# Optimization experiments

Hardware: AMD Instinct MI355X
Metric: run time of the kernel (lower is better)

Reference implementation:

```python
import jax, jax.numpy as jnp
import numpy as np

T, B, D, H = 512, 128, 512, 512

def setup_inputs() -> dict:
    key = jax.random.key(0)
    k1, k2, k3, k4 = jax.random.split(key, 4)
    s_in = 1.0 / np.sqrt(D)
    s_h = 1.0 / np.sqrt(H)
    return {
        "x": jax.random.normal(k1, (T, B, D), dtype=jnp.float32),
        "resets": jax.random.randint(k2, (T, B), 0, 2) > 0,
        "h0": jnp.zeros((B, H), dtype=jnp.float32),  # GRUCell.initialize_carry -> zeros
        "Wi": jax.random.normal(k3, (D, 3 * H), dtype=jnp.float32) * s_in,  # [ir|iz|in]
        "bi": jnp.zeros((3 * H,), dtype=jnp.float32),
        "Wh": jax.random.normal(k4, (H, 3 * H), dtype=jnp.float32) * s_h,  # [hr|hz|hn]
        "bhn": jnp.zeros((H,), dtype=jnp.float32),
    }

def reference(x, resets, h0, Wi, bi, Wh, bhn):
    # Precompute all input-side gate projections in one big GEMM: [T,B,3H]
    xg = jnp.einsum('tbd,dk->tbk', x, Wi) + bi

    def step(h, inp):
        xg_t, reset_t = inp
        # reset masking: replace carry with fresh zero carry where episode resets
        h = jnp.where(reset_t[:, None], jnp.zeros_like(h), h)
        hg = h @ Wh  # [B,3H]
        xr, xz, xn = jnp.split(xg_t, 3, axis=-1)
        hr, hz, hn = jnp.split(hg, 3, axis=-1)
        r = jax.nn.sigmoid(xr + hr)
        z = jax.nn.sigmoid(xz + hz)
        n = jnp.tanh(xn + r * (hn + bhn))
        h_new = (1.0 - z) * n + z * h
        return h_new, h_new

    h_final, ys = jax.lax.scan(step, h0, (xg, resets))
    return h_final, ys
```

## Files before the change

### kernel.cpp

```cpp
#include <hip/hip_runtime.h>

typedef __attribute__((ext_vector_type(4))) float f32x4;
typedef __attribute__((ext_vector_type(8))) _Float16 f16x8;
typedef __attribute__((ext_vector_type(4))) _Float16 f16x4;
typedef unsigned short u16;
typedef unsigned int u32;
typedef unsigned long long u64;

#define XGCAP 34304
#define TRASH (XGCAP - 1)

__device__ __forceinline__ float sigm(float v){ return 1.0f / (1.0f + __expf(-v)); }
__device__ __forceinline__ float tanh_fast(float v){
  v = fminf(15.0f, fmaxf(-15.0f, v));
  float e = __expf(2.0f * v);
  return (e - 1.0f) / (e + 1.0f);
}
__device__ __forceinline__ double aload(const double* p){
  return __hip_atomic_load(p, __ATOMIC_RELAXED, __HIP_MEMORY_SCOPE_AGENT);
}
__device__ __forceinline__ void astore64(u64* p, u64 v){
  __hip_atomic_store(p, v, __ATOMIC_RELAXED, __HIP_MEMORY_SCOPE_AGENT);
}

__global__ __launch_bounds__(512) void prep_lists(
    const void* __restrict__ resets_raw, const float* __restrict__ h0,
    u32* __restrict__ rows, u32* __restrict__ off, int* __restrict__ nlists,
    u32* __restrict__ succ, _Float16* __restrict__ hq)
{
  __shared__ u32 bitmap[2048];
  __shared__ u32 cnt[520];
  __shared__ u32 offs[521];
  __shared__ u32 cur[520];
  __shared__ int is_bytes, h0nz;
  const int tid = threadIdx.x;
  const int lane = tid & 63, wave = tid >> 6;
  for (int i = tid; i < 2048; i += 512) bitmap[i] = 0;
  for (int i = tid; i < 520; i += 512){ cnt[i] = 0; cur[i] = 0; }
  if (tid == 0){ is_bytes = 0; h0nz = 0; }
  for (int i = tid; i < 64; i += 512){ rows[65536 + i] = (2u << 16); succ[65536 + i] = TRASH; }
  __syncthreads();
  {
    const u32* w = (const u32*)resets_raw;
    int bad = 0;
    for (int i = tid; i < 4096; i += 512) bad |= (w[i] > 1u);
    if (bad) atomicOr(&is_bytes, 1);
  }
  {
    const u32* hw = (const u32*)h0;
    u32 o = 0;
    for (int i = tid; i < 65536; i += 512) o |= hw[i];
    if (o) atomicOr(&h0nz, 1);
  }
  __syncthreads();
  const bool h0zero = (h0nz == 0);
  if (is_bytes){
    const u32* wb = (const u32*)resets_raw;
    for (int i = tid; i < 16384; i += 512){
      u32 v = wb[i];
      u32 bits = ((v & 0xFFu) ? 1u : 0u) | (((v >> 8) & 0xFFu) ? 2u : 0u)
               | (((v >> 16) & 0xFFu) ? 4u : 0u) | (((v >> 24) & 0xFFu) ? 8u : 0u);
      if (bits) atomicOr(&bitmap[i >> 3], bits << ((i & 7) * 4));
    }
  } else {
    const u32* w = (const u32*)resets_raw;
    for (int r = 0; r < 128; ++r){
      u32 v = w[r * 512 + tid];
      u64 m = __ballot(v != 0u);
      if (lane == 0){
        int idx = r * 16 + wave * 2;
        bitmap[idx] = (u32)m; bitmap[idx + 1] = (u32)(m >> 32);
      }
    }
  }
  __syncthreads();
  if (tid < 128){
    const int b = tid;
    int depth = 0;
    for (int t = 0; t < 512; ++t){
      int pos = t * 128 + b;
      bool rs = (bitmap[pos >> 5] >> (pos & 31)) & 1u;
      depth = rs ? 0 : ((t == 0) ? 0 : depth + 1);
      int li = (depth == 0) ? ((rs || h0zero) ? 0 : 1) : (depth + 1);
      atomicAdd(&cnt[li], 1u);
    }
  }
  __syncthreads();
  if (tid == 0){
    u32 s = 0; int mx = 0;
    for (int i = 0; i < 520; ++i){
      offs[i] = s; s += cnt[i];
      if (cnt[i]) mx = i;
    }
    offs[520] = s;
    *nlists = mx + 1;
  }
  __syncthreads();
  for (int i = tid; i < 521; i += 512) off[i] = offs[i];
  __syncthreads();
  const u32 n0 = offs[1];
  if (tid < 128){
    const int b = tid;
    int depth = 0;
    u32 prev_p = 0;
    for (int t = 0; t < 512; ++t){
      int pos = t * 128 + b;
      bool rs = (bitmap[pos >> 5] >> (pos & 31)) & 1u;
      depth = rs ? 0 : ((t == 0) ? 0 : depth + 1);
      int li = (depth == 0) ? ((rs || h0zero) ? 0 : 1) : (depth + 1);
      u32 p = offs[li] + atomicAdd(&cur[li], 1u);
      u32 fl = rs ? 1u : ((t == 0) ? (h0zero ? 1u : 2u) : 0u);
      rows[p] = (u32)t | ((u32)b << 9) | (fl << 16);
      succ[p] = TRASH;
      if (t > 0 && !rs) succ[prev_p] = p - n0;
      prev_p = p;
    }
  }
  __syncthreads();
  if (!h0zero){
    const u32 c1 = offs[2] - offs[1];
    for (u32 idx = tid; idx < c1 * 512u; idx += 512){
      u32 lpos = offs[1] + (idx >> 9);
      u32 c = idx & 511u;
      u32 b = (rows[lpos] >> 9) & 127u;
      hq[(size_t)(lpos - n0) * 512 + c] = (_Float16)h0[(size_t)b * 512 + c];
    }
  }
}

__global__ void prep_w(const float* __restrict__ Wi, const float* __restrict__ Wh,
                       char* __restrict__ wimg, u32* __restrict__ flags)
{
  if (blockIdx.x < 64){
    #pragma unroll
    for (int i = 0; i < 4; ++i)
      flags[blockIdx.x * 1024 + (int)threadIdx.x + i * 256] = 0;
  }
  __shared__ float tile[64][65];
  const int bc = blockIdx.x % 24;
  const int bk = blockIdx.x / 24;
  const int scol0 = (bc % 3) * 512 + (bc / 3) * 64;
  const int k0 = bk * 64;
  #pragma unroll
  for (int i = 0; i < 4; ++i){
    int idx = (int)threadIdx.x + i*256;
    int kk = idx >> 4, c4 = idx & 15;
    int k = k0 + kk;
    const float* src = (k < 512) ? (Wi + (size_t)k*1536 + scol0 + c4*4)
                                 : (Wh + (size_t)(k-512)*1536 + scol0 + c4*4);
    float4 v = *(const float4*)src;
    tile[kk][c4*4+0] = v.x; tile[kk][c4*4+1] = v.y;
    tile[kk][c4*4+2] = v.z; tile[kk][c4*4+3] = v.w;
  }
  __syncthreads();
  const int jb = bc / 3;
  #pragma unroll
  for (int i = 0; i < 4; ++i){
    int idx = (int)threadIdx.x + i*256;
    int cc = idx >> 4, k4 = idx & 15;
    int cimg = (bc % 3)*64 + cc;
    f16x4 c;
    c[0] = (_Float16)tile[k4*4+0][cc]; c[1] = (_Float16)tile[k4*4+1][cc];
    c[2] = (_Float16)tile[k4*4+2][cc]; c[3] = (_Float16)tile[k4*4+3][cc];
    int bby = k4*8;
    int sb = (bby & 8) | ((bby & 0x70) ^ ((cimg & 7) << 4));
    *(f16x4*)(wimg + ((size_t)(jb*16 + bk))*24576 + cimg*128 + sb) = c;
  }
}

__global__ __launch_bounds__(256, 2) void xg_gemm(
    const float* __restrict__ x, const float* __restrict__ bi,
    const float* __restrict__ bhn, const char* __restrict__ wimg,
    _Float16* __restrict__ xg, const u32* __restrict__ rows,
    const u32* __restrict__ off, const u32* __restrict__ succ,
    _Float16* __restrict__ hq, u32* __restrict__ flags,
    float* __restrict__ out)
{
  __shared__ __align__(16) char smem[16384];
  const int tid = threadIdx.x;
  const int lane = tid & 63, wave = tid >> 6;
  const int tm = (int)blockIdx.x >> 2, jp = (int)blockIdx.x & 3;
  float* ys = out + 65536;
  const u32 n0 = off[1];

  const float* rp[4];
  #pragma unroll
  for (int i = 0; i < 4; ++i){
    u32 e = rows[tm*64 + (tid>>4) + i*16];
    rp[i] = x + ((size_t)((e & 511u)*128u + ((e >> 9) & 127u)))*512 + (tid & 15)*4;
  }

  f32x4 acc[2][3][4];
  #pragma unroll
  for (int q = 0; q < 2; ++q)
    #pragma unroll
    for (int c = 0; c < 3; ++c)
      #pragma unroll
      for (int m = 0; m < 4; ++m) acc[q][c][m] = (f32x4){0.f,0.f,0.f,0.f};

  float4 areg[4];
  #pragma unroll
  for (int i = 0; i < 4; ++i) areg[i] = *(const float4*)(rp[i]);
  #pragma unroll
  for (int i = 0; i < 4; ++i){
    int r = (tid>>4) + i*16, bby = (tid & 15)*8;
    int sb = (bby & 8) | ((bby & 0x70) ^ ((r & 7) << 4));
    f16x4 c; c[0]=(_Float16)areg[i].x; c[1]=(_Float16)areg[i].y;
             c[2]=(_Float16)areg[i].z; c[3]=(_Float16)areg[i].w;
    *(f16x4*)(smem + r*128 + sb) = c;
  }
  __syncthreads();

  for (int kc = 0; kc < 8; ++kc){
    const int cur = kc & 1;
    if (kc < 7){
      #pragma unroll
      for (int i = 0; i < 4; ++i) areg[i] = *(const float4*)(rp[i] + (kc+1)*64);
    }
    const char* Ab = smem + cur*8192;
    #pragma unroll
    for (int kk = 0; kk < 2; ++kk){
      const int bby = kk*64 + (lane>>4)*16;
      f16x8 af[4];
      #pragma unroll
      for (int mi = 0; mi < 4; ++mi){
        int rr = mi*16 + (lane & 15);
        af[mi] = *(const f16x8*)(Ab + rr*128 + (bby ^ ((rr & 7) << 4)));
      }
      #pragma unroll
      for (int jq = 0; jq < 2; ++jq){
        const char* wp = wimg + ((size_t)((jp*2 + jq)*16 + kc))*24576;
        #pragma unroll
        for (int cls = 0; cls < 3; ++cls){
          int cc = cls*64 + wave*16 + (lane & 15);
          f16x8 wf = *(const f16x8*)(wp + cc*128 + (bby ^ ((cc & 7) << 4)));
          #pragma unroll
          for (int mi = 0; mi < 4; ++mi)
            acc[jq][cls][mi] = __builtin_amdgcn_mfma_f32_16x16x32_f16(af[mi], wf, acc[jq][cls][mi], 0, 0, 0);
        }
      }
    }
    if (kc < 7){
      char* An = smem + (cur^1)*8192;
      #pragma unroll
      for (int i = 0; i < 4; ++i){
        int r = (tid>>4) + i*16, bby = (tid & 15)*8;
        int sb = (bby & 8) | ((bby & 0x70) ^ ((r & 7) << 4));
        f16x4 c; c[0]=(_Float16)areg[i].x; c[1]=(_Float16)areg[i].y;
                 c[2]=(_Float16)areg[i].z; c[3]=(_Float16)areg[i].w;
        *(f16x4*)(An + r*128 + sb) = c;
      }
    }
    __syncthreads();
  }

  const int jloc = wave*16 + (lane & 15);
  #pragma unroll
  for (int jq = 0; jq < 2; ++jq){
    const int j = (jp*2 + jq)*64 + jloc;
    const float bir = bi[j], biz = bi[512 + j], bin = bi[1024 + j], bh = bhn[j];
    #pragma unroll
    for (int mi = 0; mi < 4; ++mi){
      #pragma unroll
      for (int rg = 0; rg < 4; ++rg){
        int r = mi*16 + (lane >> 4)*4 + rg;
        u32 e = rows[tm*64 + r];
        int tt = (int)(e & 511u), bb = (int)((e >> 9) & 127u);
        float xr = acc[jq][0][mi][rg] + bir;
        float xz = acc[jq][1][mi][rg] + biz;
        float xn = acc[jq][2][mi][rg] + bin;
        if ((e >> 16) == 1u){
          float rr = sigm(xr), zz = sigm(xz);
          float nn = tanh_fast(xn + rr*bh);
          float hv = (1.f - zz)*nn;
          ys[((size_t)(tt*128 + bb))*512 + j] = hv;
          if (tt == 511) out[(size_t)bb*512 + j] = hv;
          u32 sx = succ[tm*64 + r];
          hq[(size_t)sx*512 + j] = (_Float16)hv;
        } else {
          u32 xi = (u32)(tm*64 + r) - n0;
          if (xi >= XGCAP) xi = 0;
          _Float16* p = xg + (size_t)xi*1536 + (jp*2 + jq)*192 + jloc;
          p[0]   = (_Float16)xr;
          p[64]  = (_Float16)xz;
          p[128] = (_Float16)xn;
        }
      }
    }
  }
  __syncthreads();
  if (tid < 64){
    u32 e = rows[tm*64 + tid];
    if ((e >> 16) == 1u){
      u32 fidx = (e & 511u)*128u + ((e >> 9) & 127u);
      __hip_atomic_fetch_add(&flags[fidx], 2u, __ATOMIC_RELAXED, __HIP_MEMORY_SCOPE_AGENT);
    }
  }
}

__global__ __launch_bounds__(256, 2) void gru_scan(
    const float* __restrict__ bhn, const char* __restrict__ wimg,
    const _Float16* __restrict__ xg, _Float16* __restrict__ hq,
    const u32* __restrict__ rows, const u32* __restrict__ off,
    const int* __restrict__ nlists, const u32* __restrict__ succ,
    u32* __restrict__ flags, float* __restrict__ out)
{
  __shared__ __align__(16) char smem[40960];
  float* ys = out + 65536;
  const int L = *nlists;
  const u32 n0 = off[1];
  const int tid = threadIdx.x;
  const int lane = tid & 63, wave = tid >> 6;
  const int nblk = (int)gridDim.x;
  const double* hqd = (const double*)hq;
  _Float16* hstage = (_Float16*)(smem + 32768);

  int myNext = (int)blockIdx.x;
  int gt = 0;
  for (int li = 1; li < L; ++li){
    const u32 offA = off[li];
    const int nA = (int)(off[li+1] - offA);
    const int tA = (nA + 63) >> 6;
    const int nt = tA * 8;
    while (myNext < gt + nt){
      const int tile = myNext - gt;
      myNext += nblk;
      const int tm = tile >> 3, jb = tile & 7;
      const u32 rowbase = offA + (u32)tm*64u;
      const u32 xibase = rowbase - n0;
      const int mcount = min(64, nA - tm*64);
      const char* wp = wimg + ((size_t)jb*16 + 8)*24576;
      const int jloc = wave*16 + (lane & 15);

      if (wave == 0){
        u32 e = rows[rowbase + lane];
        if (lane < mcount && (e >> 16) == 0u){
          u32 fidx = ((e & 511u) - 1u)*128u + ((e >> 9) & 127u);
          int guard = 0;
          while (__hip_atomic_load(&flags[fidx], __ATOMIC_RELAXED, __HIP_MEMORY_SCOPE_AGENT) < 8u){
            __builtin_amdgcn_s_sleep(1);
            if (++guard > (1 << 20)) break;
          }
        }
      }
      __syncthreads();

      _Float16 xgp[3][4][4];
      #pragma unroll
      for (int mi = 0; mi < 4; ++mi){
        #pragma unroll
        for (int rg = 0; rg < 4; ++rg){
          u32 xi = xibase + (u32)(mi*16 + (lane >> 4)*4 + rg);
          if (xi >= XGCAP) xi = 0;
          const _Float16* p = xg + (size_t)xi*1536 + jb*192 + jloc;
          xgp[0][mi][rg] = p[0];
          xgp[1][mi][rg] = p[64];
          xgp[2][mi][rg] = p[128];
        }
      }

      f32x4 acc[3][4];
      #pragma unroll
      for (int c = 0; c < 3; ++c)
        #pragma unroll
        for (int m = 0; m < 4; ++m) acc[c][m] = (f32x4){0.f,0.f,0.f,0.f};
      float hp[4][4];
      double s0[4], s1[4], s2[4];

#define ALOAD(S, CK) do{ \
    const double* p_ = hqd + (size_t)(xibase + (u32)(tid>>2))*128 + (CK)*16 + (tid&3)*4; \
    S[0] = aload(p_); S[1] = aload(p_+1); S[2] = aload(p_+2); S[3] = aload(p_+3); }while(0)

#define AWRITE(S, CK) do{ \
    char* An_ = smem + ((CK) & 3)*8192; \
    int r_ = tid>>2; \
    _Pragma("unroll") for (int i_ = 0; i_ < 4; ++i_){ \
      int bby_ = (tid&3)*32 + i_*8; \
      int sb_ = (bby_ & 8) | ((bby_ & 0x70) ^ ((r_ & 7) << 4)); \
      *(double*)(An_ + r_*128 + sb_) = S[i_]; } }while(0)

#define COMPUTE(KC) do{ \
    const char* Ab_ = smem + ((KC) & 3)*8192; \
    _Pragma("unroll") for (int kk_ = 0; kk_ < 2; ++kk_){ \
      const int bby_ = kk_*64 + (lane>>4)*16; \
      f16x8 af_[4]; \
      _Pragma("unroll") for (int mi_ = 0; mi_ < 4; ++mi_){ \
        int rr_ = mi_*16 + (lane & 15); \
        af_[mi_] = *(const f16x8*)(Ab_ + rr_*128 + (bby_ ^ ((rr_ & 7) << 4))); } \
      _Pragma("unroll") for (int cl_ = 0; cl_ < 3; ++cl_){ \
        int cc_ = cl_*64 + wave*16 + (lane & 15); \
        f16x8 wf_ = *(const f16x8*)(wp + (size_t)(KC)*24576 + cc_*128 + (bby_ ^ ((cc_ & 7) << 4))); \
        _Pragma("unroll") for (int mi_ = 0; mi_ < 4; ++mi_) \
          acc[cl_][mi_] = __builtin_amdgcn_mfma_f32_16x16x32_f16(af_[mi_], wf_, acc[cl_][mi_], 0, 0, 0); } } \
    if ((KC) == jb){ \
      const int bb2_ = jloc*2; \
      _Pragma("unroll") for (int mi_ = 0; mi_ < 4; ++mi_) \
        _Pragma("unroll") for (int rg_ = 0; rg_ < 4; ++rg_){ \
          int r2_ = mi_*16 + (lane >> 4)*4 + rg_; \
          int sb2_ = (bb2_ & 0x0F) | ((bb2_ & 0x70) ^ ((r2_ & 7) << 4)); \
          hp[mi_][rg_] = (float)(*(const _Float16*)(Ab_ + r2_*128 + sb2_)); } } }while(0)

      ALOAD(s0, 0); ALOAD(s1, 1); ALOAD(s2, 2);
      AWRITE(s0, 0);
      __syncthreads();
      ALOAD(s0, 3); COMPUTE(0); AWRITE(s1, 1); __syncthreads();
      ALOAD(s1, 4); COMPUTE(1); AWRITE(s2, 2); __syncthreads();
      ALOAD(s2, 5); COMPUTE(2); AWRITE(s0, 3); __syncthreads();
      ALOAD(s0, 6); COMPUTE(3); AWRITE(s1, 4); __syncthreads();
      ALOAD(s1, 7); COMPUTE(4); AWRITE(s2, 5); __syncthreads();
                    COMPUTE(5); AWRITE(s0, 6); __syncthreads();
                    COMPUTE(6); AWRITE(s1, 7); __syncthreads();
                    COMPUTE(7);
#undef ALOAD
#undef AWRITE
#undef COMPUTE

      const int j = jb*64 + jloc;
      const float bh = bhn[j];
      #pragma unroll
      for (int mi = 0; mi < 4; ++mi){
        #pragma unroll
        for (int rg = 0; rg < 4; ++rg){
          int r = mi*16 + (lane >> 4)*4 + rg;
          float rr = sigm((float)xgp[0][mi][rg] + acc[0][mi][rg]);
          float zz = sigm((float)xgp[1][mi][rg] + acc[1][mi][rg]);
          float nn = tanh_fast((float)xgp[2][mi][rg] + rr*(acc[2][mi][rg] + bh));
          float hv = (1.f - zz)*nn + zz*hp[mi][rg];
          hstage[r*64 + jloc] = (_Float16)hv;
          if (r < mcount){
            u32 e = rows[rowbase + r];
            int tt = (int)(e & 511u), bb = (int)((e >> 9) & 127u);
            ys[((size_t)(tt*128 + bb))*512 + j] = hv;
            if (tt == 511) out[(size_t)bb*512 + j] = hv;
          }
        }
      }
      __syncthreads();
      {
        int row = tid >> 2;
        if (row < mcount){
          u32 sx = succ[rowbase + row];
          const u64* src = (const u64*)(hstage + row*64) + (tid & 3)*4;
          u64* dst = (u64*)hq + (size_t)sx*128 + jb*16 + (tid & 3)*4;
          astore64(dst+0, src[0]); astore64(dst+1, src[1]);
          astore64(dst+2, src[2]); astore64(dst+3, src[3]);
        }
      }
      __syncthreads();
      if (tid < mcount){
        u32 e = rows[rowbase + tid];
        u32 fidx = (e & 511u)*128u + ((e >> 9) & 127u);
        __hip_atomic_fetch_add(&flags[fidx], 1u, __ATOMIC_RELAXED, __HIP_MEMORY_SCOPE_AGENT);
      }
    }
    gt += nt;
  }
}

extern "C" void kernel_launch(void* const* d_in, const int* in_sizes, int n_in,
                              void* d_out, int out_size, void* d_ws, size_t ws_size,
                              hipStream_t stream)
{
  const float* x  = (const float*)d_in[0];
  const void*  resets = d_in[1];
  const float* h0 = (const float*)d_in[2];
  const float* Wi = (const float*)d_in[3];
  const float* bi = (const float*)d_in[4];
  const float* Wh = (const float*)d_in[5];
  const float* bhn= (const float*)d_in[6];
  float* out = (float*)d_out;

  char* ws = (char*)d_ws;
  u32* off    = (u32*)ws;
  int* nlists = (int*)(ws + 4096);
  u32* rows   = (u32*)(ws + 8192);
  u32* flags  = (u32*)(ws + 294912);
  u32* succ   = (u32*)(ws + 589824);
  char* wimg  = ws + 917504;
  _Float16* xg = (_Float16*)(ws + 4194304);
  _Float16* hq = (_Float16*)(ws + 109576192);

  prep_lists<<<dim3(1), dim3(512), 0, stream>>>(resets, h0, rows, off, nlists, succ, hq);
  prep_w<<<dim3(384), dim3(256), 0, stream>>>(Wi, Wh, wimg, flags);
  xg_gemm<<<dim3(4096), dim3(256), 0, stream>>>(x, bi, bhn, wimg, xg, rows, off, succ, hq, flags, out);

  int perCU = 0;
  (void)hipOccupancyMaxActiveBlocksPerMultiprocessor(&perCU, gru_scan, 256, 0);
  if (perCU < 1) perCU = 1;
  int grid = perCU * 256;
  if (grid > 1024) grid = 1024;

  void* args[] = {(void*)&bhn, (void*)&wimg, (void*)&xg, (void*)&hq,
                  (void*)&rows, (void*)&off, (void*)&nlists, (void*)&succ,
                  (void*)&flags, (void*)&out};
  hipLaunchCooperativeKernel(gru_scan, dim3(grid), dim3(256), args, 0, stream);

  (void)in_sizes; (void)n_in; (void)out_size; (void)ws_size;
}
```

Before: 1.135 ms.

## Fuse input GEMM into persistent GRU scan kernel with per-row readiness flags

Merges the separate input-projection GEMM kernel into the cooperative scan kernel. Each persistent block first processes GEMM tiles in a grid-stride loop, then moves on to the scan. New per-row xflags let scan tiles wait only for the specific xg rows they need, so recurrence work can overlap the tail of the GEMM instead of waiting at a kernel boundary. It also skips hidden-state stores and flag bumps for rows with no successor. The cost is extra polling on a second flag array and possible load imbalance or spinning while GEMM tiles are still in flight.

```diff
diff --git a/kernel.cpp b/kernel.cpp
--- a/kernel.cpp
+++ b/kernel.cpp
@@ -9,6 +9,7 @@
 
 #define XGCAP 34304
 #define TRASH (XGCAP - 1)
+#define NXG 4096
 
 __device__ __forceinline__ float sigm(float v){ return 1.0f / (1.0f + __expf(-v)); }
 __device__ __forceinline__ float tanh_fast(float v){
@@ -21,6 +22,12 @@
 }
 __device__ __forceinline__ void astore64(u64* p, u64 v){
   __hip_atomic_store(p, v, __ATOMIC_RELAXED, __HIP_MEMORY_SCOPE_AGENT);
+}
+__device__ __forceinline__ u32 apoll(const u32* p){
+  return __hip_atomic_load(p, __ATOMIC_RELAXED, __HIP_MEMORY_SCOPE_AGENT);
+}
+__device__ __forceinline__ void abump(u32* p, u32 v){
+  __hip_atomic_fetch_add(p, v, __ATOMIC_RELAXED, __HIP_MEMORY_SCOPE_AGENT);
 }
 
 __global__ __launch_bounds__(512) void prep_lists(
@@ -129,12 +136,12 @@
 }
 
 __global__ void prep_w(const float* __restrict__ Wi, const float* __restrict__ Wh,
-                       char* __restrict__ wimg, u32* __restrict__ flags)
+                       char* __restrict__ wimg, u32* __restrict__ zflags)
 {
-  if (blockIdx.x < 64){
+  if (blockIdx.x < 128){
     #pragma unroll
     for (int i = 0; i < 4; ++i)
-      flags[blockIdx.x * 1024 + (int)threadIdx.x + i * 256] = 0;
+      zflags[blockIdx.x * 1024 + (int)threadIdx.x + i * 256] = 0;
   }
   __shared__ float tile[64][65];
   const int bc = blockIdx.x % 24;
@@ -168,154 +175,148 @@
   }
 }
 
-__global__ __launch_bounds__(256, 2) void xg_gemm(
+__global__ __launch_bounds__(256, 2) void gru_fused(
     const float* __restrict__ x, const float* __restrict__ bi,
     const float* __restrict__ bhn, const char* __restrict__ wimg,
-    _Float16* __restrict__ xg, const u32* __restrict__ rows,
-    const u32* __restrict__ off, const u32* __restrict__ succ,
-    _Float16* __restrict__ hq, u32* __restrict__ flags,
-    float* __restrict__ out)
-{
-  __shared__ __align__(16) char smem[16384];
-  const int tid = threadIdx.x;
-  const int lane = tid & 63, wave = tid >> 6;
-  const int tm = (int)blockIdx.x >> 2, jp = (int)blockIdx.x & 3;
-  float* ys = out + 65536;
-  const u32 n0 = off[1];
-
-  const float* rp[4];
-  #pragma unroll
-  for (int i = 0; i < 4; ++i){
-    u32 e = rows[tm*64 + (tid>>4) + i*16];
-    rp[i] = x + ((size_t)((e & 511u)*128u + ((e >> 9) & 127u)))*512 + (tid & 15)*4;
-  }
-
-  f32x4 acc[2][3][4];
-  #pragma unroll
-  for (int q = 0; q < 2; ++q)
-    #pragma unroll
-    for (int c = 0; c < 3; ++c)
-      #pragma unroll
-      for (int m = 0; m < 4; ++m) acc[q][c][m] = (f32x4){0.f,0.f,0.f,0.f};
-
-  float4 areg[4];
-  #pragma unroll
-  for (int i = 0; i < 4; ++i) areg[i] = *(const float4*)(rp[i]);
-  #pragma unroll
-  for (int i = 0; i < 4; ++i){
-    int r = (tid>>4) + i*16, bby = (tid & 15)*8;
-    int sb = (bby & 8) | ((bby & 0x70) ^ ((r & 7) << 4));
-    f16x4 c; c[0]=(_Float16)areg[i].x; c[1]=(_Float16)areg[i].y;
-             c[2]=(_Float16)areg[i].z; c[3]=(_Float16)areg[i].w;
-    *(f16x4*)(smem + r*128 + sb) = c;
-  }
-  __syncthreads();
-
-  for (int kc = 0; kc < 8; ++kc){
-    const int cur = kc & 1;
-    if (kc < 7){
-      #pragma unroll
-      for (int i = 0; i < 4; ++i) areg[i] = *(const float4*)(rp[i] + (kc+1)*64);
-    }
-    const char* Ab = smem + cur*8192;
-    #pragma unroll
-    for (int kk = 0; kk < 2; ++kk){
-      const int bby = kk*64 + (lane>>4)*16;
-      f16x8 af[4];
-      #pragma unroll
-      for (int mi = 0; mi < 4; ++mi){
-        int rr = mi*16 + (lane & 15);
-        af[mi] = *(const f16x8*)(Ab + rr*128 + (bby ^ ((rr & 7) << 4)));
-      }
-      #pragma unroll
-      for (int jq = 0; jq < 2; ++jq){
-        const char* wp = wimg + ((size_t)((jp*2 + jq)*16 + kc))*24576;
-        #pragma unroll
-        for (int cls = 0; cls < 3; ++cls){
-          int cc = cls*64 + wave*16 + (lane & 15);
-          f16x8 wf = *(const f16x8*)(wp + cc*128 + (bby ^ ((cc & 7) << 4)));
-          #pragma unroll
-          for (int mi = 0; mi < 4; ++mi)
-            acc[jq][cls][mi] = __builtin_amdgcn_mfma_f32_16x16x32_f16(af[mi], wf, acc[jq][cls][mi], 0, 0, 0);
-        }
-      }
-    }
-    if (kc < 7){
-      char* An = smem + (cur^1)*8192;
-      #pragma unroll
-      for (int i = 0; i < 4; ++i){
-        int r = (tid>>4) + i*16, bby = (tid & 15)*8;
-        int sb = (bby & 8) | ((bby & 0x70) ^ ((r & 7) << 4));
-        f16x4 c; c[0]=(_Float16)areg[i].x; c[1]=(_Float16)areg[i].y;
-                 c[2]=(_Float16)areg[i].z; c[3]=(_Float16)areg[i].w;
-        *(f16x4*)(An + r*128 + sb) = c;
-      }
-    }
-    __syncthreads();
-  }
-
-  const int jloc = wave*16 + (lane & 15);
-  #pragma unroll
-  for (int jq = 0; jq < 2; ++jq){
-    const int j = (jp*2 + jq)*64 + jloc;
-    const float bir = bi[j], biz = bi[512 + j], bin = bi[1024 + j], bh = bhn[j];
-    #pragma unroll
-    for (int mi = 0; mi < 4; ++mi){
-      #pragma unroll
-      for (int rg = 0; rg < 4; ++rg){
-        int r = mi*16 + (lane >> 4)*4 + rg;
-        u32 e = rows[tm*64 + r];
-        int tt = (int)(e & 511u), bb = (int)((e >> 9) & 127u);
-        float xr = acc[jq][0][mi][rg] + bir;
-        float xz = acc[jq][1][mi][rg] + biz;
-        float xn = acc[jq][2][mi][rg] + bin;
-        if ((e >> 16) == 1u){
-          float rr = sigm(xr), zz = sigm(xz);
-          float nn = tanh_fast(xn + rr*bh);
-          float hv = (1.f - zz)*nn;
-          ys[((size_t)(tt*128 + bb))*512 + j] = hv;
-          if (tt == 511) out[(size_t)bb*512 + j] = hv;
-          u32 sx = succ[tm*64 + r];
-          hq[(size_t)sx*512 + j] = (_Float16)hv;
-        } else {
-          u32 xi = (u32)(tm*64 + r) - n0;
-          if (xi >= XGCAP) xi = 0;
-          _Float16* p = xg + (size_t)xi*1536 + (jp*2 + jq)*192 + jloc;
-          p[0]   = (_Float16)xr;
-          p[64]  = (_Float16)xz;
-          p[128] = (_Float16)xn;
-        }
-      }
-    }
-  }
-  __syncthreads();
-  if (tid < 64){
-    u32 e = rows[tm*64 + tid];
-    if ((e >> 16) == 1u){
-      u32 fidx = (e & 511u)*128u + ((e >> 9) & 127u);
-      __hip_atomic_fetch_add(&flags[fidx], 2u, __ATOMIC_RELAXED, __HIP_MEMORY_SCOPE_AGENT);
-    }
-  }
-}
-
-__global__ __launch_bounds__(256, 2) void gru_scan(
-    const float* __restrict__ bhn, const char* __restrict__ wimg,
-    const _Float16* __restrict__ xg, _Float16* __restrict__ hq,
+    _Float16* __restrict__ xg, _Float16* __restrict__ hq,
     const u32* __restrict__ rows, const u32* __restrict__ off,
     const int* __restrict__ nlists, const u32* __restrict__ succ,
-    u32* __restrict__ flags, float* __restrict__ out)
+    u32* __restrict__ hflags, u32* __restrict__ xflags,
+    float* __restrict__ out)
 {
   __shared__ __align__(16) char smem[40960];
   float* ys = out + 65536;
-  const int L = *nlists;
   const u32 n0 = off[1];
   const int tid = threadIdx.x;
   const int lane = tid & 63, wave = tid >> 6;
   const int nblk = (int)gridDim.x;
+
+  int g = (int)blockIdx.x;
+  while (g < NXG){
+    const int tm = g >> 2, jp = g & 3;
+    g += nblk;
+
+    const float* rp[4];
+    #pragma unroll
+    for (int i = 0; i < 4; ++i){
+      u32 e = rows[tm*64 + (tid>>4) + i*16];
+      rp[i] = x + ((size_t)((e & 511u)*128u + ((e >> 9) & 127u)))*512 + (tid & 15)*4;
+    }
+
+    f32x4 acc[2][3][4];
+    #pragma unroll
+    for (int q = 0; q < 2; ++q)
+      #pragma unroll
+      for (int c = 0; c < 3; ++c)
+        #pragma unroll
+        for (int m = 0; m < 4; ++m) acc[q][c][m] = (f32x4){0.f,0.f,0.f,0.f};
+
+    float4 areg[4];
+    #pragma unroll
+    for (int i = 0; i < 4; ++i) areg[i] = *(const float4*)(rp[i]);
+    #pragma unroll
+    for (int i = 0; i < 4; ++i){
+      int r = (tid>>4) + i*16, bby = (tid & 15)*8;
+      int sb = (bby & 8) | ((bby & 0x70) ^ ((r & 7) << 4));
+      f16x4 c; c[0]=(_Float16)areg[i].x; c[1]=(_Float16)areg[i].y;
+               c[2]=(_Float16)areg[i].z; c[3]=(_Float16)areg[i].w;
+      *(f16x4*)(smem + r*128 + sb) = c;
+    }
+    __syncthreads();
+
+    for (int kc = 0; kc < 8; ++kc){
+      const int cur = kc & 1;
+      if (kc < 7){
+        #pragma unroll
+        for (int i = 0; i < 4; ++i) areg[i] = *(const float4*)(rp[i] + (kc+1)*64);
+      }
+      const char* Ab = smem + cur*8192;
+      #pragma unroll
+      for (int kk = 0; kk < 2; ++kk){
+        const int bby = kk*64 + (lane>>4)*16;
+        f16x8 af[4];
+        #pragma unroll
+        for (int mi = 0; mi < 4; ++mi){
+          int rr = mi*16 + (lane & 15);
+          af[mi] = *(const f16x8*)(Ab + rr*128 + (bby ^ ((rr & 7) << 4)));
+        }
+        #pragma unroll
+        for (int jq = 0; jq < 2; ++jq){
+          const char* wp = wimg + ((size_t)((jp*2 + jq)*16 + kc))*24576;
+          #pragma unroll
+          for (int cls = 0; cls < 3; ++cls){
+            int cc = cls*64 + wave*16 + (lane & 15);
+            f16x8 wf = *(const f16x8*)(wp + cc*128 + (bby ^ ((cc & 7) << 4)));
+            #pragma unroll
+            for (int mi = 0; mi < 4; ++mi)
+              acc[jq][cls][mi] = __builtin_amdgcn_mfma_f32_16x16x32_f16(af[mi], wf, acc[jq][cls][mi], 0, 0, 0);
+          }
+        }
+      }
+      if (kc < 7){
+        char* An = smem + (cur^1)*8192;
+        #pragma unroll
+        for (int i = 0; i < 4; ++i){
+          int r = (tid>>4) + i*16, bby = (tid & 15)*8;
+          int sb = (bby & 8) | ((bby & 0x70) ^ ((r & 7) << 4));
+          f16x4 c; c[0]=(_Float16)areg[i].x; c[1]=(_Float16)areg[i].y;
+                   c[2]=(_Float16)areg[i].z; c[3]=(_Float16)areg[i].w;
+          *(f16x4*)(An + r*128 + sb) = c;
+        }
+      }
+      __syncthreads();
+    }
+
+    const int jloc = wave*16 + (lane & 15);
+    #pragma unroll
+    for (int jq = 0; jq < 2; ++jq){
+      const int j = (jp*2 + jq)*64 + jloc;
+      const float bir = bi[j], biz = bi[512 + j], bin = bi[1024 + j], bh = bhn[j];
+      #pragma unroll
+      for (int mi = 0; mi < 4; ++mi){
+        #pragma unroll
+        for (int rg = 0; rg < 4; ++rg){
+          int r = mi*16 + (lane >> 4)*4 + rg;
+          u32 e = rows[tm*64 + r];
+          int tt = (int)(e & 511u), bb = (int)((e >> 9) & 127u);
+          float xr = acc[jq][0][mi][rg] + bir;
+          float xz = acc[jq][1][mi][rg] + biz;
+          float xn = acc[jq][2][mi][rg] + bin;
+          if ((e >> 16) == 1u){
+            float rr = sigm(xr), zz = sigm(xz);
+            float nn = tanh_fast(xn + rr*bh);
+            float hv = (1.f - zz)*nn;
+            ys[((size_t)(tt*128 + bb))*512 + j] = hv;
+            if (tt == 511) out[(size_t)bb*512 + j] = hv;
+            u32 sx = succ[tm*64 + r];
+            hq[(size_t)sx*512 + j] = (_Float16)hv;
+          } else {
+            u32 xi = (u32)(tm*64 + r) - n0;
+            if (xi >= XGCAP) xi = 0;
+            _Float16* p = xg + (size_t)xi*1536 + (jp*2 + jq)*192 + jloc;
+            p[0]   = (_Float16)xr;
+            p[64]  = (_Float16)xz;
+            p[128] = (_Float16)xn;
+          }
+        }
+      }
+    }
+    __syncthreads();
+    if (tid < 64){
+      u32 e = rows[tm*64 + tid];
+      if ((e >> 16) == 1u){
+        abump(&hflags[(e & 511u)*128u + ((e >> 9) & 127u)], 2u);
+      } else {
+        abump(&xflags[tm*64 + tid], 1u);
+      }
+    }
+    __syncthreads();
+  }
+
+  const int L = *nlists;
   const double* hqd = (const double*)hq;
   _Float16* hstage = (_Float16*)(smem + 32768);
-
-  int myNext = (int)blockIdx.x;
+  int myNext = g - NXG;
   int gt = 0;
   for (int li = 1; li < L; ++li){
     const u32 offA = off[li];
@@ -332,15 +333,17 @@
       const char* wp = wimg + ((size_t)jb*16 + 8)*24576;
       const int jloc = wave*16 + (lane & 15);
 
-      if (wave == 0){
+      if (wave == 0 && lane < mcount){
         u32 e = rows[rowbase + lane];
-        if (lane < mcount && (e >> 16) == 0u){
-          u32 fidx = ((e & 511u) - 1u)*128u + ((e >> 9) & 127u);
-          int guard = 0;
-          while (__hip_atomic_load(&flags[fidx], __ATOMIC_RELAXED, __HIP_MEMORY_SCOPE_AGENT) < 8u){
-            __builtin_amdgcn_s_sleep(1);
-            if (++guard > (1 << 20)) break;
-          }
+        const bool needH = ((e >> 16) == 0u);
+        u32 hidx = ((e & 511u) - 1u)*128u + ((e >> 9) & 127u);
+        int guard = 0;
+        for (;;){
+          bool ok = apoll(&xflags[rowbase + lane]) >= 4u;
+          if (ok && needH) ok = apoll(&hflags[hidx]) >= 8u;
+          if (ok) break;
+          __builtin_amdgcn_s_sleep(1);
+          if (++guard > (1 << 20)) break;
         }
       }
       __syncthreads();
@@ -440,17 +443,18 @@
         int row = tid >> 2;
         if (row < mcount){
           u32 sx = succ[rowbase + row];
-          const u64* src = (const u64*)(hstage + row*64) + (tid & 3)*4;
-          u64* dst = (u64*)hq + (size_t)sx*128 + jb*16 + (tid & 3)*4;
-          astore64(dst+0, src[0]); astore64(dst+1, src[1]);
-          astore64(dst+2, src[2]); astore64(dst+3, src[3]);
+          if (sx != TRASH){
+            const u64* src = (const u64*)(hstage + row*64) + (tid & 3)*4;
+            u64* dst = (u64*)hq + (size_t)sx*128 + jb*16 + (tid & 3)*4;
+            astore64(dst+0, src[0]); astore64(dst+1, src[1]);
+            astore64(dst+2, src[2]); astore64(dst+3, src[3]);
+          }
         }
       }
       __syncthreads();
-      if (tid < mcount){
+      if (tid < mcount && succ[rowbase + tid] != TRASH){
         u32 e = rows[rowbase + tid];
-        u32 fidx = (e & 511u)*128u + ((e >> 9) & 127u);
-        __hip_atomic_fetch_add(&flags[fidx], 1u, __ATOMIC_RELAXED, __HIP_MEMORY_SCOPE_AGENT);
+        abump(&hflags[(e & 511u)*128u + ((e >> 9) & 127u)], 1u);
       }
     }
     gt += nt;
@@ -474,26 +478,27 @@
   u32* off    = (u32*)ws;
   int* nlists = (int*)(ws + 4096);
   u32* rows   = (u32*)(ws + 8192);
-  u32* flags  = (u32*)(ws + 294912);
-  u32* succ   = (u32*)(ws + 589824);
-  char* wimg  = ws + 917504;
-  _Float16* xg = (_Float16*)(ws + 4194304);
-  _Float16* hq = (_Float16*)(ws + 109576192);
+  u32* hflags = (u32*)(ws + 294912);
+  u32* xflags = (u32*)(ws + 557056);
+  u32* succ   = (u32*)(ws + 819200);
+  char* wimg  = ws + 1081600;
+  _Float16* xg = (_Float16*)(ws + 4325376);
+  _Float16* hq = (_Float16*)(ws + 109707264);
 
   prep_lists<<<dim3(1), dim3(512), 0, stream>>>(resets, h0, rows, off, nlists, succ, hq);
-  prep_w<<<dim3(384), dim3(256), 0, stream>>>(Wi, Wh, wimg, flags);
-  xg_gemm<<<dim3(4096), dim3(256), 0, stream>>>(x, bi, bhn, wimg, xg, rows, off, succ, hq, flags, out);
+  prep_w<<<dim3(384), dim3(256), 0, stream>>>(Wi, Wh, wimg, hflags);
 
   int perCU = 0;
-  (void)hipOccupancyMaxActiveBlocksPerMultiprocessor(&perCU, gru_scan, 256, 0);
+  (void)hipOccupancyMaxActiveBlocksPerMultiprocessor(&perCU, gru_fused, 256, 0);
   if (perCU < 1) perCU = 1;
   int grid = perCU * 256;
   if (grid > 1024) grid = 1024;
 
-  void* args[] = {(void*)&bhn, (void*)&wimg, (void*)&xg, (void*)&hq,
-                  (void*)&rows, (void*)&off, (void*)&nlists, (void*)&succ,
-                  (void*)&flags, (void*)&out};
-  hipLaunchCooperativeKernel(gru_scan, dim3(grid), dim3(256), args, 0, stream);
+  void* args[] = {(void*)&x, (void*)&bi, (void*)&bhn, (void*)&wimg,
+                  (void*)&xg, (void*)&hq, (void*)&rows, (void*)&off,
+                  (void*)&nlists, (void*)&succ, (void*)&hflags, (void*)&xflags,
+                  (void*)&out};
+  hipLaunchCooperativeKernel(gru_fused, dim3(grid), dim3(256), args, 0, stream);
 
   (void)in_sizes; (void)n_in; (void)out_size; (void)ws_size;
 }
```

New measurement: 1.106 ms. -2.6%, faster.
